# Kernel optimization log

Hardware: AMD Instinct MI355X
Metric: run time of the kernel (lower is better)

Reference implementation:

```python
import jax, jax.numpy as jnp
import numpy as np

NUM_FEATURES = 1024
GRID_SIZE = 5
SPLINE_ORDER = 3
GRID_RANGE = (-2.0, 2.0)
LN_EPS = 1e-5
DEN_EPS = 1e-7


def build_grid(num_features, grid_size, spline_order, grid_range):
    start, end = float(grid_range[0]), float(grid_range[1])
    step = (end - start) / grid_size
    base = jnp.linspace(start - spline_order * step, end + spline_order * step,
                        grid_size + 2 * spline_order + 1, dtype=jnp.float32)
    return jnp.broadcast_to(base[None, :], (num_features, base.shape[0]))


def setup_inputs() -> dict:
    key = jax.random.key(0)
    k_x, k_w = jax.random.split(key)
    x = jax.random.normal(k_x, (8192, NUM_FEATURES), dtype=jnp.float32)
    ln_weight = jnp.ones((NUM_FEATURES,), jnp.float32)
    ln_bias = jnp.zeros((NUM_FEATURES,), jnp.float32)
    # torch init: uniform_(-0.1, 0.1)
    spline_weight = jax.random.uniform(k_w, (NUM_FEATURES, GRID_SIZE + SPLINE_ORDER),
                                       minval=-0.1, maxval=0.1, dtype=jnp.float32)
    base_weight = jnp.ones((NUM_FEATURES,), jnp.float32)
    grid = build_grid(NUM_FEATURES, GRID_SIZE, SPLINE_ORDER, GRID_RANGE)
    return {"x": x, "ln_weight": ln_weight, "ln_bias": ln_bias,
            "spline_weight": spline_weight, "base_weight": base_weight, "grid": grid}


def layer_norm(x, w, b):
    mu = jnp.mean(x, axis=-1, keepdims=True)
    var = jnp.mean((x - mu) ** 2, axis=-1, keepdims=True)
    return (x - mu) * jax.lax.rsqrt(var + LN_EPS) * w + b


def b_splines(x, grid, spline_order):
    # x: (B, F); grid: (F, K). Cox-de Boor recursion, unrolled over fixed order.
    xe = x[:, :, None]                      # (B, F, 1)
    g = grid[None, :, :]                    # (1, F, K)
    bases = ((xe >= g[:, :, :-1]) & (xe < g[:, :, 1:])).astype(x.dtype)
    # right-endpoint correction: x == grid[:, -1] belongs to the last interval
    right_mask = x == grid[None, :, -1]
    bases = bases.at[:, :, -1].set(jnp.where(right_mask, jnp.asarray(1.0, x.dtype), bases[:, :, -1]))
    for k in range(1, spline_order + 1):
        left_den = g[:, :, k:-1] - g[:, :, :-(k + 1)]
        left_ok = jnp.abs(left_den) > DEN_EPS
        left_den_safe = jnp.where(left_ok, left_den, jnp.asarray(1.0, x.dtype))
        left = jnp.where(left_ok, (xe - g[:, :, :-(k + 1)]) / left_den_safe * bases[:, :, :-1], 0.0)
        right_den = g[:, :, k + 1:] - g[:, :, 1:-k]
        right_ok = jnp.abs(right_den) > DEN_EPS
        right_den_safe = jnp.where(right_ok, right_den, jnp.asarray(1.0, x.dtype))
        right = jnp.where(right_ok, (g[:, :, k + 1:] - xe) / right_den_safe * bases[:, :, 1:], 0.0)
        bases = left + right
    return bases                            # (B, F, grid_size + spline_order)


def reference(x, ln_weight, ln_bias, spline_weight, base_weight, grid):
    orig_shape = x.shape
    xf = x.reshape(-1, NUM_FEATURES)
    normed = layer_norm(xf, ln_weight, ln_bias)
    bases = b_splines(normed, grid, SPLINE_ORDER)
    spline_out = jnp.einsum('bfk,fk->bf', bases, spline_weight)
    residual = base_weight[None, :] * jax.nn.silu(normed)
    return (spline_out + residual).reshape(orig_shape)
```

## Files before the change

### kernel.cpp

```cpp
#include <hip/hip_runtime.h>
#include <hip/hip_bf16.h>


#define F 1024
#define BLOCK 512
#define WPB 8
#define NBLOCKS 1024

__device__ __forceinline__ float bf2f(unsigned short u) {
    union { unsigned int i; float f; } v;
    v.i = ((unsigned int)u) << 16;
    return v.f;
}

__device__ __forceinline__ unsigned short f2bf(float f) {
    union { float f; unsigned int i; } v;
    v.f = f;
    unsigned int x = v.i;
    unsigned int r = (x + 0x7FFFu + ((x >> 16) & 1u)) >> 16;
    return (unsigned short)r;
}

template <bool BF16>
__device__ __forceinline__ float ldv(const void* p, int i) {
    if constexpr (BF16) return bf2f(((const unsigned short*)p)[i]);
    else                return ((const float*)p)[i];
}

template <bool BF16>
__device__ __forceinline__ void stv(void* p, int i, float v) {
    if constexpr (BF16) ((unsigned short*)p)[i] = f2bf(v);
    else                ((float*)p)[i] = v;
}

template <bool BF16>
__device__ __forceinline__ void kan_body(
    const void* __restrict__ x,   const void* __restrict__ lnw,
    const void* __restrict__ lnb, const void* __restrict__ sw,
    const void* __restrict__ bw,  const void* __restrict__ grid,
    void* __restrict__ out, int rows,
    float* s_w, float* s_p)
{
    const int tid  = threadIdx.x;
    const int wave = tid >> 6;
    const int lane = tid & 63;

    for (int i = tid; i < F * 8; i += BLOCK) {
        int f = i >> 3, k = i & 7;
        s_w[k * F + f] = ldv<BF16>(sw, i);
    }
    for (int f = tid; f < F; f += BLOCK) {
        s_p[4 * f + 0] = ldv<BF16>(lnw, f);
        s_p[4 * f + 1] = ldv<BF16>(lnb, f);
        s_p[4 * f + 2] = ldv<BF16>(bw,  f);
        s_p[4 * f + 3] = 0.0f;
    }
    const float g0   = ldv<BF16>(grid, 0);
    const float g11  = ldv<BF16>(grid, 11);
    const float invh = 11.0f / (g11 - g0);

    __syncthreads();

    for (int row = blockIdx.x * WPB + wave; row < rows; row += gridDim.x * WPB) {
        const int rbase = row * F;

        float xv[16];
        float s = 0.0f, s2 = 0.0f;
        #pragma unroll
        for (int j = 0; j < 16; ++j) {
            xv[j] = ldv<BF16>(x, rbase + lane + 64 * j);
            s  += xv[j];
            s2 += xv[j] * xv[j];
        }
        #pragma unroll
        for (int off = 32; off > 0; off >>= 1) {
            s  += __shfl_xor(s,  off, 64);
            s2 += __shfl_xor(s2, off, 64);
        }
        const float mu   = s * (1.0f / F);
        const float rstd = rsqrtf(s2 * (1.0f / F) - mu * mu + 1e-5f);

        #pragma unroll
        for (int j = 0; j < 16; ++j) {
            const int f = lane + 64 * j;

            const float4 pp = *reinterpret_cast<const float4*>(&s_p[4 * f]);
            float t = (xv[j] - mu) * rstd * pp.x + pp.y;

            float sig = 1.0f / (1.0f + __expf(-t));
            float res = pp.z * t * sig;

            float ttn = (t - g0) * invh;
            int j0 = (int)floorf(ttn);
            j0 = j0 < 0 ? 0 : (j0 > 10 ? 10 : j0);
            float u  = ttn - (float)j0;
            float u2 = u * u, u3 = u2 * u;
            float om = 1.0f - u;
            float N0 = om * om * om * (1.0f / 6.0f);
            float N3 = u3 * (1.0f / 6.0f);
            float N1 = (1.0f / 6.0f) * (4.0f - 6.0f * u2 + 3.0f * u3);
            float N2 = 1.0f - N0 - N1 - N3;
            float Nv[4] = { N0, N1, N2, N3 };

            float sp = 0.0f;
            #pragma unroll
            for (int r = 0; r < 4; ++r) {
                int jj = j0 - 3 + r;
                int jc = jj < 0 ? 0 : (jj > 7 ? 7 : jj);
                float wv = s_w[jc * F + f];
                sp += (jj == jc) ? wv * Nv[r] : 0.0f;
            }
            sp = (t >= g0 && t <= g11) ? sp : 0.0f;

            stv<BF16>(out, rbase + f, sp + res);
        }
    }
}

__global__ __launch_bounds__(BLOCK, 4) void kan_kernel(
    const void* __restrict__ x,   const void* __restrict__ lnw,
    const void* __restrict__ lnb, const void* __restrict__ sw,
    const void* __restrict__ bw,  const void* __restrict__ grid,
    void* __restrict__ out, int rows)
{
    __shared__ float s_w[8 * F];
    __shared__ float s_p[4 * F];

    const float g = ((const float*)grid)[0];
    const bool is_bf16 = !(g > -4.45f && g < -4.35f);

    if (is_bf16) kan_body<true >(x, lnw, lnb, sw, bw, grid, out, rows, s_w, s_p);
    else         kan_body<false>(x, lnw, lnb, sw, bw, grid, out, rows, s_w, s_p);
}

extern "C" void kernel_launch(void* const* d_in, const int* in_sizes, int n_in,
                              void* d_out, int out_size, void* d_ws, size_t ws_size,
                              hipStream_t stream) {
    const void* x    = d_in[0];
    const void* lnw  = d_in[1];
    const void* lnb  = d_in[2];
    const void* sw   = d_in[3];
    const void* bw   = d_in[4];
    const void* grid = d_in[5];

    int rows = in_sizes[0] / F;
    int nblk = (rows + WPB - 1) / WPB;
    if (nblk > NBLOCKS) nblk = NBLOCKS;
    if (nblk < 1) nblk = 1;

    kan_kernel<<<dim3(nblk), dim3(BLOCK), 0, stream>>>(
        x, lnw, lnb, sw, bw, grid, d_out, rows);
}
```

Baseline: 105.8 us.

## Vectorize row loads/stores with XOR-swizzled LDS layout and halve grid

Switches global loads and stores to 128-bit vector accesses (float4 or int4 of bf16), with each lane owning contiguous features. To avoid LDS bank conflicts from the new strided per-lane access, spline weights and per-feature params are stored with an XOR swizzle, and the float4-packed param array is split into separate arrays. The grid is capped at 512 blocks, with the loop stride now using a compile-time constant. The aim is fewer memory instructions and better coalescing on a bandwidth-bound kernel, at the risk of more LDS address arithmetic and fewer resident blocks.

```diff
diff --git a/kernel.cpp b/kernel.cpp
--- a/kernel.cpp
+++ b/kernel.cpp
@@ -5,7 +5,7 @@
 #define F 1024
 #define BLOCK 512
 #define WPB 8
-#define NBLOCKS 1024
+#define GRID 512
 
 __device__ __forceinline__ float bf2f(unsigned short u) {
     union { unsigned int i; float f; } v;
@@ -27,10 +27,39 @@
     else                return ((const float*)p)[i];
 }
 
-template <bool BF16>
-__device__ __forceinline__ void stv(void* p, int i, float v) {
-    if constexpr (BF16) ((unsigned short*)p)[i] = f2bf(v);
-    else                ((float*)p)[i] = v;
+__device__ __forceinline__ float kan_elem(
+    float xval, float mu, float rstd, int sf,
+    const float* __restrict__ s_w,   const float* __restrict__ s_lnw,
+    const float* __restrict__ s_lnb, const float* __restrict__ s_bw,
+    float g0, float g11, float invh)
+{
+    float t = (xval - mu) * rstd * s_lnw[sf] + s_lnb[sf];
+
+    float sig = 1.0f / (1.0f + __expf(-t));
+    float res = s_bw[sf] * t * sig;
+
+    float ttn = (t - g0) * invh;
+    int j0 = (int)floorf(ttn);
+    j0 = j0 < 0 ? 0 : (j0 > 10 ? 10 : j0);
+    float u  = ttn - (float)j0;
+    float u2 = u * u, u3 = u2 * u;
+    float om = 1.0f - u;
+    float N0 = om * om * om * (1.0f / 6.0f);
+    float N3 = u3 * (1.0f / 6.0f);
+    float N1 = (1.0f / 6.0f) * (4.0f - 6.0f * u2 + 3.0f * u3);
+    float N2 = 1.0f - N0 - N1 - N3;
+    float Nv[4] = { N0, N1, N2, N3 };
+
+    float sp = 0.0f;
+    #pragma unroll
+    for (int r = 0; r < 4; ++r) {
+        int jj = j0 - 3 + r;
+        int jc = jj < 0 ? 0 : (jj > 7 ? 7 : jj);
+        float wv = s_w[jc * F + sf];
+        sp += (jj == jc) ? wv * Nv[r] : 0.0f;
+    }
+    sp = (t >= g0 && t <= g11) ? sp : 0.0f;
+    return sp + res;
 }
 
 template <bool BF16>
@@ -39,21 +68,23 @@
     const void* __restrict__ lnb, const void* __restrict__ sw,
     const void* __restrict__ bw,  const void* __restrict__ grid,
     void* __restrict__ out, int rows,
-    float* s_w, float* s_p)
+    float* s_w, float* s_lnw, float* s_lnb, float* s_bw)
 {
+    constexpr int SWM = BF16 ? 7 : 3;
     const int tid  = threadIdx.x;
     const int wave = tid >> 6;
     const int lane = tid & 63;
 
     for (int i = tid; i < F * 8; i += BLOCK) {
         int f = i >> 3, k = i & 7;
-        s_w[k * F + f] = ldv<BF16>(sw, i);
+        int sf = f ^ ((f >> 5) & SWM);
+        s_w[k * F + sf] = ldv<BF16>(sw, i);
     }
     for (int f = tid; f < F; f += BLOCK) {
-        s_p[4 * f + 0] = ldv<BF16>(lnw, f);
-        s_p[4 * f + 1] = ldv<BF16>(lnb, f);
-        s_p[4 * f + 2] = ldv<BF16>(bw,  f);
-        s_p[4 * f + 3] = 0.0f;
+        int sf = f ^ ((f >> 5) & SWM);
+        s_lnw[sf] = ldv<BF16>(lnw, f);
+        s_lnb[sf] = ldv<BF16>(lnb, f);
+        s_bw[sf]  = ldv<BF16>(bw,  f);
     }
     const float g0   = ldv<BF16>(grid, 0);
     const float g11  = ldv<BF16>(grid, 11);
@@ -61,58 +92,80 @@
 
     __syncthreads();
 
-    for (int row = blockIdx.x * WPB + wave; row < rows; row += gridDim.x * WPB) {
+    for (int row = blockIdx.x * WPB + wave; row < rows; row += GRID * WPB) {
         const int rbase = row * F;
 
-        float xv[16];
-        float s = 0.0f, s2 = 0.0f;
-        #pragma unroll
-        for (int j = 0; j < 16; ++j) {
-            xv[j] = ldv<BF16>(x, rbase + lane + 64 * j);
-            s  += xv[j];
-            s2 += xv[j] * xv[j];
-        }
-        #pragma unroll
-        for (int off = 32; off > 0; off >>= 1) {
-            s  += __shfl_xor(s,  off, 64);
-            s2 += __shfl_xor(s2, off, 64);
-        }
-        const float mu   = s * (1.0f / F);
-        const float rstd = rsqrtf(s2 * (1.0f / F) - mu * mu + 1e-5f);
-
-        #pragma unroll
-        for (int j = 0; j < 16; ++j) {
-            const int f = lane + 64 * j;
-
-            const float4 pp = *reinterpret_cast<const float4*>(&s_p[4 * f]);
-            float t = (xv[j] - mu) * rstd * pp.x + pp.y;
-
-            float sig = 1.0f / (1.0f + __expf(-t));
-            float res = pp.z * t * sig;
-
-            float ttn = (t - g0) * invh;
-            int j0 = (int)floorf(ttn);
-            j0 = j0 < 0 ? 0 : (j0 > 10 ? 10 : j0);
-            float u  = ttn - (float)j0;
-            float u2 = u * u, u3 = u2 * u;
-            float om = 1.0f - u;
-            float N0 = om * om * om * (1.0f / 6.0f);
-            float N3 = u3 * (1.0f / 6.0f);
-            float N1 = (1.0f / 6.0f) * (4.0f - 6.0f * u2 + 3.0f * u3);
-            float N2 = 1.0f - N0 - N1 - N3;
-            float Nv[4] = { N0, N1, N2, N3 };
-
-            float sp = 0.0f;
-            #pragma unroll
-            for (int r = 0; r < 4; ++r) {
-                int jj = j0 - 3 + r;
-                int jc = jj < 0 ? 0 : (jj > 7 ? 7 : jj);
-                float wv = s_w[jc * F + f];
-                sp += (jj == jc) ? wv * Nv[r] : 0.0f;
-            }
-            sp = (t >= g0 && t <= g11) ? sp : 0.0f;
-
-            stv<BF16>(out, rbase + f, sp + res);
+        if constexpr (!BF16) {
+            const float4* xr = (const float4*)((const float*)x + rbase);
+            float4 xv[4];
+            float s = 0.0f, s2 = 0.0f;
+            #pragma unroll
+            for (int q = 0; q < 4; ++q) {
+                xv[q] = xr[lane + 64 * q];
+                s  += xv[q].x + xv[q].y + xv[q].z + xv[q].w;
+                s2 += xv[q].x * xv[q].x + xv[q].y * xv[q].y
+                    + xv[q].z * xv[q].z + xv[q].w * xv[q].w;
+            }
+            #pragma unroll
+            for (int off = 32; off > 0; off >>= 1) {
+                s  += __shfl_xor(s,  off, 64);
+                s2 += __shfl_xor(s2, off, 64);
+            }
+            const float mu   = s * (1.0f / F);
+            const float rstd = rsqrtf(s2 * (1.0f / F) - mu * mu + 1e-5f);
+
+            const int xm = (lane >> 3) & 3;
+            float4* op = (float4*)((float*)out + rbase);
+            #pragma unroll
+            for (int q = 0; q < 4; ++q) {
+                const int fb = 4 * lane + 256 * q;
+                float4 o;
+                o.x = kan_elem(xv[q].x, mu, rstd, fb + (0 ^ xm), s_w, s_lnw, s_lnb, s_bw, g0, g11, invh);
+                o.y = kan_elem(xv[q].y, mu, rstd, fb + (1 ^ xm), s_w, s_lnw, s_lnb, s_bw, g0, g11, invh);
+                o.z = kan_elem(xv[q].z, mu, rstd, fb + (2 ^ xm), s_w, s_lnw, s_lnb, s_bw, g0, g11, invh);
+                o.w = kan_elem(xv[q].w, mu, rstd, fb + (3 ^ xm), s_w, s_lnw, s_lnb, s_bw, g0, g11, invh);
+                op[lane + 64 * q] = o;
+            }
+        } else {
+            const int4* xr = (const int4*)((const unsigned short*)x + rbase);
+            int4 xi[2];
+            float xv[16];
+            float s = 0.0f, s2 = 0.0f;
+            #pragma unroll
+            for (int q = 0; q < 2; ++q) {
+                xi[q] = xr[lane + 64 * q];
+                const unsigned short* us = (const unsigned short*)&xi[q];
+                #pragma unroll
+                for (int c = 0; c < 8; ++c) {
+                    float v = bf2f(us[c]);
+                    xv[8 * q + c] = v;
+                    s  += v;
+                    s2 += v * v;
+                }
+            }
+            #pragma unroll
+            for (int off = 32; off > 0; off >>= 1) {
+                s  += __shfl_xor(s,  off, 64);
+                s2 += __shfl_xor(s2, off, 64);
+            }
+            const float mu   = s * (1.0f / F);
+            const float rstd = rsqrtf(s2 * (1.0f / F) - mu * mu + 1e-5f);
+
+            const int xm = (lane >> 2) & 7;
+            int4* op = (int4*)((unsigned short*)out + rbase);
+            #pragma unroll
+            for (int q = 0; q < 2; ++q) {
+                const int fb = 8 * lane + 512 * q;
+                int4 ov;
+                unsigned short* ou = (unsigned short*)&ov;
+                #pragma unroll
+                for (int c = 0; c < 8; ++c) {
+                    float r = kan_elem(xv[8 * q + c], mu, rstd, fb + (c ^ xm),
+                                       s_w, s_lnw, s_lnb, s_bw, g0, g11, invh);
+                    ou[c] = f2bf(r);
+                }
+                op[lane + 64 * q] = ov;
+            }
         }
     }
 }
@@ -124,13 +177,15 @@
     void* __restrict__ out, int rows)
 {
     __shared__ float s_w[8 * F];
-    __shared__ float s_p[4 * F];
+    __shared__ float s_lnw[F];
+    __shared__ float s_lnb[F];
+    __shared__ float s_bw[F];
 
     const float g = ((const float*)grid)[0];
     const bool is_bf16 = !(g > -4.45f && g < -4.35f);
 
-    if (is_bf16) kan_body<true >(x, lnw, lnb, sw, bw, grid, out, rows, s_w, s_p);
-    else         kan_body<false>(x, lnw, lnb, sw, bw, grid, out, rows, s_w, s_p);
+    if (is_bf16) kan_body<true >(x, lnw, lnb, sw, bw, grid, out, rows, s_w, s_lnw, s_lnb, s_bw);
+    else         kan_body<false>(x, lnw, lnb, sw, bw, grid, out, rows, s_w, s_lnw, s_lnb, s_bw);
 }
 
 extern "C" void kernel_launch(void* const* d_in, const int* in_sizes, int n_in,
@@ -145,7 +200,7 @@
 
     int rows = in_sizes[0] / F;
     int nblk = (rows + WPB - 1) / WPB;
-    if (nblk > NBLOCKS) nblk = NBLOCKS;
+    if (nblk > GRID) nblk = GRID;
     if (nblk < 1) nblk = 1;
 
     kan_kernel<<<dim3(nblk), dim3(BLOCK), 0, stream>>>(
```

After: 101.9 us. 3.7% less time.
